# Kernel optimization log

Hardware: AMD Instinct MI355X
Metric: run time of the kernel (lower is better)

## Reference

```python
import jax, jax.numpy as jnp
import numpy as np

def setup_inputs() -> dict:
    key = jax.random.key(0)
    ks = jax.random.split(key, 8)
    b, n, dim = 2, 2048, 512
    h, d, K, M = 8, 64, 32, 131072
    x = jax.random.normal(ks[0], (b, n, dim), dtype=jnp.float32)
    mem_db = jax.random.normal(ks[1], (b, M, 2, d), dtype=jnp.float32)
    knn_idx = jax.random.randint(ks[2], (b, h, n, K), 0, M)
    mem_mask = jax.random.randint(ks[3], (b, h, n, K), 0, 2).astype(bool)
    Wq = jax.random.normal(ks[4], (h * d, dim), dtype=jnp.float32) * 0.02
    Wkv = jax.random.normal(ks[5], (2 * d, dim), dtype=jnp.float32) * 0.02
    Wout = jax.random.normal(ks[6], (dim, h * d), dtype=jnp.float32) * 0.02
    scale_param = jnp.ones((h, 1, 1), dtype=jnp.float32) * np.log(20.0)
    return {"x": x, "mem_db": mem_db, "knn_idx": knn_idx, "mem_mask": mem_mask,
            "Wq": Wq, "Wkv": Wkv, "Wout": Wout, "scale_param": scale_param}

def reference(x, mem_db, knn_idx, mem_mask, Wq, Wkv, Wout, scale_param):
    b, n, dim = x.shape
    h = scale_param.shape[0]
    d = Wq.shape[0] // h
    # projections
    q = jnp.einsum('bnc,ec->bne', x, Wq).reshape(b, n, h, d).transpose(0, 2, 1, 3)  # b h n d
    q = q / jnp.linalg.norm(q, axis=-1, keepdims=True).clip(1e-12)  # l2norm
    kv = jnp.einsum('bnc,ec->bne', x, Wkv)  # [b,n,2d]; detached + added to memory (side effect only)
    scale = jnp.exp(scale_param)  # [h,1,1]
    # per-query KNN gather: mem_db [b,M,2,d], knn_idx [b,h,n,K] -> [b,h,n,K,2,d]
    mem_kv = jax.vmap(lambda db, ix: db[ix])(mem_db, knn_idx)
    mem_k = mem_kv[..., 0, :]  # b h n K d
    mem_v = mem_kv[..., 1, :]
    sim = jnp.einsum('bhid,bhijd->bhij', q, mem_k) * scale  # b h n K
    mask_value = -jnp.finfo(sim.dtype).max
    sim = jnp.where(mem_mask, sim, mask_value)
    attn = jax.nn.softmax(sim, axis=-1)  # stable softmax
    out = jnp.einsum('bhij,bhijd->bhid', attn, mem_v)  # b h n d
    out = out.transpose(0, 2, 1, 3).reshape(b, n, h * d)
    return jnp.einsum('bne,ce->bnc', out, Wout)
```

## Files before the change

### kernel.cpp

```cpp
#include <hip/hip_runtime.h>
#include <hip/hip_bf16.h>
#include <math.h>

#define B_SZ 2
#define N_SEQ 2048
#define DIM 512
#define H_HEADS 8
#define D_HEAD 64
#define K_NN 32
#define M_DB 131072

typedef __attribute__((ext_vector_type(8))) short bf16x8;
typedef __attribute__((ext_vector_type(4))) float f32x4;

__global__ void detect_mask_layout(const unsigned char* __restrict__ mb,
                                   int* __restrict__ flag) {
    int t = threadIdx.x;
    unsigned char v = 0;
    for (int e = t; e < 1024; e += 64) {
        v |= mb[4 * e + 1];
        v |= mb[4 * e + 2];
        v |= mb[4 * e + 3];
    }
    unsigned long long any = __ballot(v != 0);
    if (t == 0) *flag = (any != 0ull) ? 1 : 0;
}

__device__ __forceinline__ void cvt_hi_lo(float f, short& h, short& l) {
    unsigned u = __float_as_uint(f);
    unsigned uh = u + (0x7fffu + ((u >> 16) & 1u));
    h = (short)(uh >> 16);
    float r = f - __uint_as_float((uh >> 16) << 16);
    unsigned ur = __float_as_uint(r);
    l = (short)((ur + (0x7fffu + ((ur >> 16) & 1u))) >> 16);
}

__device__ __forceinline__ void load_frag_split(const float* __restrict__ p,
                                                bf16x8& h, bf16x8& l) {
    float4 f0 = *(const float4*)p;
    float4 f1 = *(const float4*)(p + 4);
    float ff[8] = {f0.x, f0.y, f0.z, f0.w, f1.x, f1.y, f1.z, f1.w};
#pragma unroll
    for (int e = 0; e < 8; ++e) {
        short hh, ll;
        cvt_hi_lo(ff[e], hh, ll);
        h[e] = hh; l[e] = ll;
    }
}

__global__ __launch_bounds__(256) void gemm_mfma_f32(
    const float* __restrict__ A, const float* __restrict__ W,
    float* __restrict__ C, int Mdim, int Ndim, int Kdim)
{
    const int t = threadIdx.x;
    const int wave = t >> 6, lane = t & 63;
    const int r = lane & 15, qd = lane >> 4;
    const int m0 = blockIdx.x * 64 + (wave & 1) * 32;
    const int n0 = blockIdx.y * 64 + (wave >> 1) * 32;

    f32x4 acc[2][2];
#pragma unroll
    for (int i = 0; i < 2; ++i)
#pragma unroll
        for (int j = 0; j < 2; ++j) acc[i][j] = (f32x4){0.f, 0.f, 0.f, 0.f};

    const float* pa0 = A + (size_t)(m0 + r) * Kdim + qd * 8;
    const float* pa1 = pa0 + (size_t)16 * Kdim;
    const float* pb0 = W + (size_t)(n0 + r) * Kdim + qd * 8;
    const float* pb1 = pb0 + (size_t)16 * Kdim;

    for (int k0 = 0; k0 < Kdim; k0 += 32) {
        bf16x8 ah0, al0, ah1, al1, bh0, bl0, bh1, bl1;
        load_frag_split(pa0 + k0, ah0, al0);
        load_frag_split(pa1 + k0, ah1, al1);
        load_frag_split(pb0 + k0, bh0, bl0);
        load_frag_split(pb1 + k0, bh1, bl1);

        acc[0][0] = __builtin_amdgcn_mfma_f32_16x16x32_bf16(ah0, bh0, acc[0][0], 0, 0, 0);
        acc[0][1] = __builtin_amdgcn_mfma_f32_16x16x32_bf16(ah0, bh1, acc[0][1], 0, 0, 0);
        acc[1][0] = __builtin_amdgcn_mfma_f32_16x16x32_bf16(ah1, bh0, acc[1][0], 0, 0, 0);
        acc[1][1] = __builtin_amdgcn_mfma_f32_16x16x32_bf16(ah1, bh1, acc[1][1], 0, 0, 0);

        acc[0][0] = __builtin_amdgcn_mfma_f32_16x16x32_bf16(ah0, bl0, acc[0][0], 0, 0, 0);
        acc[0][1] = __builtin_amdgcn_mfma_f32_16x16x32_bf16(ah0, bl1, acc[0][1], 0, 0, 0);
        acc[1][0] = __builtin_amdgcn_mfma_f32_16x16x32_bf16(ah1, bl0, acc[1][0], 0, 0, 0);
        acc[1][1] = __builtin_amdgcn_mfma_f32_16x16x32_bf16(ah1, bl1, acc[1][1], 0, 0, 0);

        acc[0][0] = __builtin_amdgcn_mfma_f32_16x16x32_bf16(al0, bh0, acc[0][0], 0, 0, 0);
        acc[0][1] = __builtin_amdgcn_mfma_f32_16x16x32_bf16(al0, bh1, acc[0][1], 0, 0, 0);
        acc[1][0] = __builtin_amdgcn_mfma_f32_16x16x32_bf16(al1, bh0, acc[1][0], 0, 0, 0);
        acc[1][1] = __builtin_amdgcn_mfma_f32_16x16x32_bf16(al1, bh1, acc[1][1], 0, 0, 0);
    }

#pragma unroll
    for (int mt = 0; mt < 2; ++mt)
#pragma unroll
        for (int nt = 0; nt < 2; ++nt)
#pragma unroll
            for (int rr = 0; rr < 4; ++rr)
                C[(size_t)(m0 + mt * 16 + qd * 4 + rr) * Ndim + n0 + nt * 16 + r] =
                    acc[mt][nt][rr];
}

__global__ __launch_bounds__(256) void attn_kernel(
    const float* __restrict__ qbuf,
    const float* __restrict__ mem_db,
    const int* __restrict__ knn_idx,
    const void* __restrict__ mem_mask,
    const float* __restrict__ scale_param,
    const int* __restrict__ flag,
    float* __restrict__ outbuf)
{
    const int wave = blockIdx.x * 4 + (threadIdx.x >> 6);
    const int lane = threadIdx.x & 63;
    const int sub = lane & 15, grp = lane >> 4;
    const int i = wave % N_SEQ;
    const int bh = wave / N_SEQ;
    const int hi = bh % H_HEADS;
    const int bi = bh / H_HEADS;

    const int bytelayout = *flag;

    const float* qrow = qbuf + (size_t)(bi * N_SEQ + i) * DIM + hi * D_HEAD;
    float qv = qrow[lane];
    float ss = qv * qv;
#pragma unroll
    for (int s = 32; s; s >>= 1) ss += __shfl_xor(ss, s);
    qv = qv / fmaxf(sqrtf(ss), 1e-12f);

    float q4[4];
#pragma unroll
    for (int c = 0; c < 4; ++c) q4[c] = __shfl(qv, 4 * sub + c);

    const float scale = __expf(scale_param[hi]);

    const size_t kb = ((size_t)(bi * H_HEADS + hi) * N_SEQ + i) * K_NN;
    int idxv = 0, maskv = 0;
    if (lane < K_NN) {
        idxv = knn_idx[kb + lane];
        if (bytelayout)
            maskv = ((const unsigned char*)mem_mask)[kb + lane] ? 1 : 0;
        else
            maskv = ((const int*)mem_mask)[kb + lane] ? 1 : 0;
    }

    const float* dbb = mem_db + (size_t)bi * M_DB * (2 * D_HEAD);

    float4 kk[8], vv[8];
#pragma unroll
    for (int g = 0; g < 8; ++g) {
        int idx = __shfl(idxv, 4 * g + grp);
        const float* row = dbb + (size_t)idx * (2 * D_HEAD);
        kk[g] = *(const float4*)(row + 4 * sub);
        vv[g] = *(const float4*)(row + D_HEAD + 4 * sub);
    }

    float s8[8];
#pragma unroll
    for (int g = 0; g < 8; ++g) {
        float p = q4[0] * kk[g].x + q4[1] * kk[g].y + q4[2] * kk[g].z + q4[3] * kk[g].w;
        p += __shfl_xor(p, 1);
        p += __shfl_xor(p, 2);
        p += __shfl_xor(p, 4);
        p += __shfl_xor(p, 8);
        s8[g] = p;
    }

    float simlane = -INFINITY;
#pragma unroll
    for (int g = 0; g < 8; ++g) {
        float tv = __shfl(s8[g], (lane & 3) << 4);
        if ((lane >> 2) == g) simlane = tv;
    }
    if (lane < K_NN)
        simlane = maskv ? simlane * scale : -3.402823466e38f;

    float m = simlane;
#pragma unroll
    for (int s = 32; s; s >>= 1) m = fmaxf(m, __shfl_xor(m, s));
    float w = __expf(simlane - m);
    float l = w;
#pragma unroll
    for (int s = 32; s; s >>= 1) l += __shfl_xor(l, s);
    float winv = w / l;

    float4 o = {0.f, 0.f, 0.f, 0.f};
#pragma unroll
    for (int g = 0; g < 8; ++g) {
        float wg = __shfl(winv, 4 * g + grp);
        o.x = fmaf(wg, vv[g].x, o.x);
        o.y = fmaf(wg, vv[g].y, o.y);
        o.z = fmaf(wg, vv[g].z, o.z);
        o.w = fmaf(wg, vv[g].w, o.w);
    }
#pragma unroll
    for (int s = 16; s <= 32; s <<= 1) {
        o.x += __shfl_xor(o.x, s);
        o.y += __shfl_xor(o.y, s);
        o.z += __shfl_xor(o.z, s);
        o.w += __shfl_xor(o.w, s);
    }
    if (grp == 0)
        *(float4*)(outbuf + (size_t)(bi * N_SEQ + i) * DIM + hi * D_HEAD + 4 * sub) = o;
}

extern "C" void kernel_launch(void* const* d_in, const int* in_sizes, int n_in,
                              void* d_out, int out_size, void* d_ws, size_t ws_size,
                              hipStream_t stream) {
    const float* x        = (const float*)d_in[0];
    const float* mem_db   = (const float*)d_in[1];
    const int*   knn_idx  = (const int*)d_in[2];
    const void*  mem_mask = d_in[3];
    const float* Wq       = (const float*)d_in[4];
    const float* Wout     = (const float*)d_in[6];
    const float* scale_p  = (const float*)d_in[7];
    float* out = (float*)d_out;

    const int Mrows = B_SZ * N_SEQ;
    const int n_x   = Mrows * DIM;

    char* ws = (char*)d_ws;
    int* flag = (int*)ws;
    float* qbuf     = (float*)(ws + 256);
    float* attn_out = qbuf + (size_t)n_x;

    detect_mask_layout<<<1, 64, 0, stream>>>((const unsigned char*)mem_mask, flag);

    dim3 ggrid(Mrows / 64, DIM / 64);
    gemm_mfma_f32<<<ggrid, 256, 0, stream>>>(x, Wq, qbuf, Mrows, DIM, DIM);

    const int n_waves = B_SZ * H_HEADS * N_SEQ;
    attn_kernel<<<n_waves / 4, 256, 0, stream>>>(qbuf, mem_db, knn_idx, mem_mask,
                                                 scale_p, flag, attn_out);

    gemm_mfma_f32<<<ggrid, 256, 0, stream>>>(attn_out, Wout, out, Mrows, DIM, DIM);
}
```

Measured before the change: 309.3 us.

## Pre-split weights to bf16 hi/lo and skip gathers for masked neighbors

Adds a kernel that converts Wq and Wout once per call into bf16 hi/lo arrays, so the GEMM loads ready-made B fragments and no longer splits them inside its loop. In the attention kernel, key/value rows for masked neighbors are redirected to row 0 of the memory database, so the random gathers collapse onto one cached line. Value rows are still gathered when every neighbor is masked, which keeps the uniform-softmax result. The cost is an extra launch and workspace for the split weights, plus some extra address logic.

```diff
diff --git a/kernel.cpp b/kernel.cpp
--- a/kernel.cpp
+++ b/kernel.cpp
@@ -48,8 +48,29 @@
     }
 }
 
+__global__ __launch_bounds__(256) void split_weights(
+    const float4* __restrict__ wq, const float4* __restrict__ wout,
+    ushort4* __restrict__ qhi, ushort4* __restrict__ qlo,
+    ushort4* __restrict__ ohi, ushort4* __restrict__ olo) {
+    const int n4 = DIM * DIM / 4;
+    int i = blockIdx.x * 256 + threadIdx.x;
+    const float4* src = (i < n4) ? wq : wout;
+    ushort4* dh = (i < n4) ? qhi : ohi;
+    ushort4* dl = (i < n4) ? qlo : olo;
+    int j = (i < n4) ? i : i - n4;
+    float4 a = src[j];
+    ushort4 h, l;
+    short hh, ll;
+    cvt_hi_lo(a.x, hh, ll); h.x = hh; l.x = ll;
+    cvt_hi_lo(a.y, hh, ll); h.y = hh; l.y = ll;
+    cvt_hi_lo(a.z, hh, ll); h.z = hh; l.z = ll;
+    cvt_hi_lo(a.w, hh, ll); h.w = hh; l.w = ll;
+    dh[j] = h; dl[j] = l;
+}
+
 __global__ __launch_bounds__(256) void gemm_mfma_f32(
-    const float* __restrict__ A, const float* __restrict__ W,
+    const float* __restrict__ A,
+    const unsigned short* __restrict__ Bhi, const unsigned short* __restrict__ Blo,
     float* __restrict__ C, int Mdim, int Ndim, int Kdim)
 {
     const int t = threadIdx.x;
@@ -66,15 +87,17 @@
 
     const float* pa0 = A + (size_t)(m0 + r) * Kdim + qd * 8;
     const float* pa1 = pa0 + (size_t)16 * Kdim;
-    const float* pb0 = W + (size_t)(n0 + r) * Kdim + qd * 8;
-    const float* pb1 = pb0 + (size_t)16 * Kdim;
+    const size_t b0 = (size_t)(n0 + r) * Kdim + qd * 8;
+    const size_t b1 = b0 + (size_t)16 * Kdim;
 
     for (int k0 = 0; k0 < Kdim; k0 += 32) {
-        bf16x8 ah0, al0, ah1, al1, bh0, bl0, bh1, bl1;
+        bf16x8 ah0, al0, ah1, al1;
         load_frag_split(pa0 + k0, ah0, al0);
         load_frag_split(pa1 + k0, ah1, al1);
-        load_frag_split(pb0 + k0, bh0, bl0);
-        load_frag_split(pb1 + k0, bh1, bl1);
+        bf16x8 bh0 = *(const bf16x8*)(Bhi + b0 + k0);
+        bf16x8 bh1 = *(const bf16x8*)(Bhi + b1 + k0);
+        bf16x8 bl0 = *(const bf16x8*)(Blo + b0 + k0);
+        bf16x8 bl1 = *(const bf16x8*)(Blo + b1 + k0);
 
         acc[0][0] = __builtin_amdgcn_mfma_f32_16x16x32_bf16(ah0, bh0, acc[0][0], 0, 0, 0);
         acc[0][1] = __builtin_amdgcn_mfma_f32_16x16x32_bf16(ah0, bh1, acc[0][1], 0, 0, 0);
@@ -144,15 +167,20 @@
             maskv = ((const int*)mem_mask)[kb + lane] ? 1 : 0;
     }
 
+    unsigned long long mbits = __ballot(maskv != 0);
+    const bool allmasked = (mbits == 0ull);
+
     const float* dbb = mem_db + (size_t)bi * M_DB * (2 * D_HEAD);
 
     float4 kk[8], vv[8];
 #pragma unroll
     for (int g = 0; g < 8; ++g) {
         int idx = __shfl(idxv, 4 * g + grp);
-        const float* row = dbb + (size_t)idx * (2 * D_HEAD);
-        kk[g] = *(const float4*)(row + 4 * sub);
-        vv[g] = *(const float4*)(row + D_HEAD + 4 * sub);
+        bool mrow = (mbits >> (4 * g + grp)) & 1ull;
+        size_t koff = mrow ? (size_t)idx * (2 * D_HEAD) : 0;
+        size_t voff = (mrow || allmasked) ? (size_t)idx * (2 * D_HEAD) : 0;
+        kk[g] = *(const float4*)(dbb + koff + 4 * sub);
+        vv[g] = *(const float4*)(dbb + voff + D_HEAD + 4 * sub);
     }
 
     float s8[8];
@@ -218,20 +246,28 @@
 
     const int Mrows = B_SZ * N_SEQ;
     const int n_x   = Mrows * DIM;
+    const int n_w   = DIM * DIM;
 
     char* ws = (char*)d_ws;
     int* flag = (int*)ws;
     float* qbuf     = (float*)(ws + 256);
     float* attn_out = qbuf + (size_t)n_x;
+    unsigned short* wq_hi = (unsigned short*)(attn_out + (size_t)n_x);
+    unsigned short* wq_lo = wq_hi + n_w;
+    unsigned short* wo_hi = wq_lo + n_w;
+    unsigned short* wo_lo = wo_hi + n_w;
 
     detect_mask_layout<<<1, 64, 0, stream>>>((const unsigned char*)mem_mask, flag);
+    split_weights<<<2 * n_w / 1024, 256, 0, stream>>>(
+        (const float4*)Wq, (const float4*)Wout,
+        (ushort4*)wq_hi, (ushort4*)wq_lo, (ushort4*)wo_hi, (ushort4*)wo_lo);
 
     dim3 ggrid(Mrows / 64, DIM / 64);
-    gemm_mfma_f32<<<ggrid, 256, 0, stream>>>(x, Wq, qbuf, Mrows, DIM, DIM);
+    gemm_mfma_f32<<<ggrid, 256, 0, stream>>>(x, wq_hi, wq_lo, qbuf, Mrows, DIM, DIM);
 
     const int n_waves = B_SZ * H_HEADS * N_SEQ;
     attn_kernel<<<n_waves / 4, 256, 0, stream>>>(qbuf, mem_db, knn_idx, mem_mask,
                                                  scale_p, flag, attn_out);
 
-    gemm_mfma_f32<<<ggrid, 256, 0, stream>>>(attn_out, Wout, out, Mrows, DIM, DIM);
-}
+    gemm_mfma_f32<<<ggrid, 256, 0, stream>>>(attn_out, wo_hi, wo_lo, out, Mrows, DIM, DIM);
+}
```

After: 288.8 us. 1.07x faster.
